# Performance work log

Hardware: AMD Instinct MI355X
Metric: run time of the kernel (lower is better)

The kernel has to match this reference:

```python
import jax, jax.numpy as jnp
import numpy as np

TOP_K = 30
NUM_RBF = 16
MAXREL = 32


def _normalize(x, eps=1e-12):
    return x / jnp.maximum(jnp.linalg.norm(x, axis=-1, keepdims=True), eps)


def gather_edges(edges, idx):
    # edges [B,L,L,C], idx [B,L,K] -> [B,L,K,C]
    return jnp.take_along_axis(edges, idx[..., None], axis=2)


def gather_nodes(nodes, idx):
    # nodes [B,L,C], idx [B,L,K] -> [B,L,K,C]
    B, L, K = idx.shape
    flat = idx.reshape(B, L * K)
    g = jnp.take_along_axis(nodes, flat[:, :, None], axis=1)
    return g.reshape(B, L, K, nodes.shape[-1])


def _rbf(D):
    mu = jnp.linspace(2.0, 22.0, NUM_RBF)
    sigma = (22.0 - 2.0) / NUM_RBF
    return jnp.exp(-(((D[..., None] - mu) / sigma) ** 2))


def _get_rbf(A, B, E_idx):
    D = jnp.sqrt(jnp.sum((A[:, :, None, :] - B[:, None, :, :]) ** 2, -1) + 1e-6)
    Dn = gather_edges(D[..., None], E_idx)[..., 0]
    return _rbf(Dn)


def _dist(X, mask, eps=1e-6):
    mask2 = mask[:, None, :] * mask[:, :, None]
    dX = X[:, None, :, :] - X[:, :, None, :]
    D = mask2 * jnp.sqrt(jnp.sum(dX ** 2, -1) + eps)
    D_max = jnp.max(D, -1, keepdims=True)
    D_adjust = D + (1.0 - mask2) * D_max
    k = min(TOP_K, X.shape[1])
    neg_vals, E_idx = jax.lax.top_k(-D_adjust, k)  # smallest-k distances
    D_neighbors = -neg_vals
    mask_neighbors = gather_edges(mask2[..., None], E_idx)
    return D_neighbors, E_idx, mask_neighbors


def _quaternions(R):
    # R [B,L,K,3,3] -> Q [B,L,K,4]
    diag = jnp.diagonal(R, axis1=-2, axis2=-1)
    Rxx, Ryy, Rzz = diag[..., 0], diag[..., 1], diag[..., 2]
    magnitudes = 0.5 * jnp.sqrt(jnp.abs(1.0 + jnp.stack(
        [Rxx - Ryy - Rzz, -Rxx + Ryy - Rzz, -Rxx - Ryy + Rzz], -1)))
    signs = jnp.sign(jnp.stack([
        R[..., 2, 1] - R[..., 1, 2],
        R[..., 0, 2] - R[..., 2, 0],
        R[..., 1, 0] - R[..., 0, 1]], -1))
    xyz = signs * magnitudes
    w = jnp.sqrt(jax.nn.relu(1.0 + jnp.sum(diag, -1, keepdims=True))) / 2.0
    Q = jnp.concatenate((xyz, w), -1)
    return _normalize(Q)


def _orientations_coarse(X, E_idx, eps=1e-6):
    dX = X[:, 1:, :] - X[:, :-1, :]
    dX_norm = jnp.linalg.norm(dX, axis=-1)
    dX_mask = ((dX_norm > 3.6) & (dX_norm < 4.0)).astype(X.dtype)
    dX = dX * dX_mask[:, :, None]
    U = _normalize(dX)
    u_2, u_1, u_0 = U[:, :-2, :], U[:, 1:-1, :], U[:, 2:, :]
    n_2 = _normalize(jnp.cross(u_2, u_1))
    n_1 = _normalize(jnp.cross(u_1, u_0))
    cosA = jnp.clip(-(u_1 * u_0).sum(-1), -1 + eps, 1 - eps)
    A = jnp.arccos(cosA)
    cosD = jnp.clip((n_2 * n_1).sum(-1), -1 + eps, 1 - eps)
    Dang = jnp.sign((u_2 * n_1).sum(-1)) * jnp.arccos(cosD)
    AD = jnp.stack((jnp.cos(A), jnp.sin(A) * jnp.cos(Dang),
                    jnp.sin(A) * jnp.sin(Dang)), -1)
    AD = jnp.pad(AD, ((0, 0), (1, 2), (0, 0)))  # [B,L,3]
    o_1 = _normalize(u_2 - u_1)
    O = jnp.stack((o_1, n_2, jnp.cross(o_1, n_2)), -2)  # [B,L-3,3,3]
    O = O.reshape(O.shape[0], O.shape[1], 9)
    O = jnp.pad(O, ((0, 0), (1, 2), (0, 0)))  # [B,L,9]
    O_nb = gather_nodes(O, E_idx).reshape(E_idx.shape[0], E_idx.shape[1], E_idx.shape[2], 3, 3)
    X_nb = gather_nodes(X, E_idx)
    Om = O.reshape(O.shape[0], O.shape[1], 3, 3)
    dXn = X_nb - X[:, :, None, :]
    dU = _normalize(jnp.einsum('blij,blkj->blki', Om, dXn))
    R = jnp.einsum('blji,blkjm->blkim', Om, O_nb)  # O^T @ O_neighbors
    Q = _quaternions(R)
    return AD, jnp.concatenate((dU, Q), -1)  # [B,L,3], [B,L,K,7]


def _forward(Ca, mask, residue_idx, chain_labels, pos_W, pos_b, edge_W, ln_g, ln_b):
    D_neighbors, E_idx, mask_neighbors = _dist(Ca, mask)
    Ca_0 = jnp.pad(Ca[:, :-1, :], ((0, 0), (1, 0), (0, 0)))
    Ca_1 = Ca
    Ca_2 = jnp.pad(Ca[:, 1:, :], ((0, 0), (0, 1), (0, 0)))
    V, O_features = _orientations_coarse(Ca, E_idx)
    RBF_all = jnp.concatenate([
        _rbf(D_neighbors),
        _get_rbf(Ca_0, Ca_0, E_idx),
        _get_rbf(Ca_2, Ca_2, E_idx),
        _get_rbf(Ca_0, Ca_1, E_idx),
        _get_rbf(Ca_0, Ca_2, E_idx),
        _get_rbf(Ca_1, Ca_0, E_idx),
        _get_rbf(Ca_1, Ca_2, E_idx),
        _get_rbf(Ca_2, Ca_0, E_idx),
        _get_rbf(Ca_2, Ca_1, E_idx)], -1)  # [B,L,K,144]
    offset = residue_idx[:, :, None] - residue_idx[:, None, :]
    offset = gather_edges(offset[..., None], E_idx)[..., 0]
    d_chains = (chain_labels[:, :, None] - chain_labels[:, None, :] == 0).astype(jnp.int32)
    E_chains = gather_edges(d_chains[..., None], E_idx)[..., 0]
    d = jnp.clip(offset + MAXREL, 0, 2 * MAXREL) * E_chains + (1 - E_chains) * (2 * MAXREL + 1)
    d_onehot = jax.nn.one_hot(d, 2 * MAXREL + 2, dtype=pos_W.dtype)
    E_positional = d_onehot @ pos_W + pos_b
    E = jnp.concatenate((E_positional, RBF_all, O_features), -1)  # [B,L,K,167]
    E = E @ edge_W  # no bias
    mu = jnp.mean(E, -1, keepdims=True)
    var = jnp.var(E, -1, keepdims=True)
    E = (E - mu) / jnp.sqrt(var + 1e-5) * ln_g + ln_b
    return E, E_idx


def setup_inputs() -> dict:
    key = jax.random.key(0)
    k1, k2, k3 = jax.random.split(key, 3)
    B, L = 2, 4096
    Ca = jax.random.normal(k1, (B, L, 3), dtype=jnp.float32) * 10.0
    mask = jnp.ones((B, L), dtype=jnp.float32)
    residue_idx = jnp.arange(B * L, dtype=jnp.int32).reshape(B, L) % L
    chain_labels = jnp.zeros((B, L), dtype=jnp.int32)
    pos_W = jax.random.normal(k2, (2 * MAXREL + 2, 16), dtype=jnp.float32) * 0.1
    pos_b = jnp.zeros((16,), dtype=jnp.float32)
    edge_in = 16 + NUM_RBF * 9 + 7  # 167
    edge_W = jax.random.normal(k3, (edge_in, 128), dtype=jnp.float32) * 0.05
    ln_g = jnp.ones((128,), dtype=jnp.float32)
    ln_b = jnp.zeros((128,), dtype=jnp.float32)
    return {"Ca": Ca, "mask": mask, "residue_idx": residue_idx,
            "chain_labels": chain_labels, "pos_W": pos_W, "pos_b": pos_b,
            "edge_W": edge_W, "ln_g": ln_g, "ln_b": ln_b}


def reference(Ca, mask, residue_idx, chain_labels, pos_W, pos_b, edge_W, ln_g, ln_b):
    return _forward(Ca, mask, residue_idx, chain_labels, pos_W, pos_b, edge_W, ln_g, ln_b)
```

## Files before the change

### kernel.cpp

```cpp
#include <hip/hip_runtime.h>
#include <math.h>

constexpr int Lc   = 4096;
constexpr int Bc   = 2;
constexpr int KNB  = 30;
constexpr int NF   = 167;
constexpr int NC   = 128;
constexpr int KP   = 200;
constexpr int NKT  = 6;
constexpr int CAP  = 512;

typedef __attribute__((ext_vector_type(8))) short bf16x8;
typedef __attribute__((ext_vector_type(4))) float f32x4;

struct V3 { float x, y, z; };

__device__ __forceinline__ float sgnf(float v) {
    return (v > 0.f) ? 1.f : ((v < 0.f) ? -1.f : 0.f);
}
__device__ __forceinline__ unsigned long long umin64(unsigned long long a, unsigned long long b) {
    return a < b ? a : b;
}
__device__ __forceinline__ void splitbf(float v, unsigned short& h, unsigned short& l) {
    unsigned u = __float_as_uint(v);
    h = (unsigned short)(u >> 16);
    float fh = __uint_as_float((unsigned)h << 16);
    l = (unsigned short)(__float_as_uint(v - fh) >> 16);
}
__device__ __forceinline__ unsigned cvtpk(float a, float b) {
    unsigned r;
    asm("v_cvt_pk_bf16_f32 %0, %1, %2" : "=v"(r) : "v"(a), "v"(b));
    return r;
}

__device__ __forceinline__ V3 unit_seg(float dx, float dy, float dz) {
    float n = sqrtf(dx * dx + dy * dy + dz * dz);
    float m = (n > 3.6f && n < 4.0f) ? 1.f : 0.f;
    float nn = fmaxf(m * n, 1e-12f);
    V3 r; r.x = dx * m / nn; r.y = dy * m / nn; r.z = dz * m / nn;
    return r;
}

__global__ __launch_bounds__(256) void topk_prep_kernel(
    const float* __restrict__ Ca, const float* __restrict__ mask,
    float* __restrict__ EidxF, int* __restrict__ EidxI,
    float* __restrict__ O, const float* __restrict__ W,
    unsigned short* __restrict__ Wh, unsigned short* __restrict__ Wl,
    int rows) {
    const int t = threadIdx.x;

    if (blockIdx.x >= rows) {
        int pb = blockIdx.x - rows;
        if (pb < 32) {
            int idx = pb * 256 + t;
            if (idx >= Bc * Lc) return;
            int b = idx >> 12, l = idx & (Lc - 1);
            float* o = O + (size_t)idx * 9;
            if (l < 1 || l >= Lc - 2) {
#pragma unroll
                for (int q = 0; q < 9; ++q) o[q] = 0.f;
                return;
            }
            const float* C = Ca + ((size_t)b * Lc + (l - 1)) * 3;
            V3 u2 = unit_seg(C[3] - C[0], C[4] - C[1], C[5] - C[2]);
            V3 u1 = unit_seg(C[6] - C[3], C[7] - C[4], C[8] - C[5]);
            float nx = u2.y * u1.z - u2.z * u1.y;
            float ny = u2.z * u1.x - u2.x * u1.z;
            float nz = u2.x * u1.y - u2.y * u1.x;
            float nn = fmaxf(sqrtf(nx * nx + ny * ny + nz * nz), 1e-12f);
            nx /= nn; ny /= nn; nz /= nn;
            float ox = u2.x - u1.x, oy = u2.y - u1.y, oz = u2.z - u1.z;
            float on = fmaxf(sqrtf(ox * ox + oy * oy + oz * oz), 1e-12f);
            ox /= on; oy /= on; oz /= on;
            o[0] = ox; o[1] = oy; o[2] = oz;
            o[3] = nx; o[4] = ny; o[5] = nz;
            o[6] = oy * nz - oz * ny;
            o[7] = oz * nx - ox * nz;
            o[8] = ox * ny - oy * nx;
        } else {
            int tt = (pb - 32) * 256 + t;
            if (tt >= NKT * 8 * 64) return;
            int lane = tt & 63, nt = (tt >> 6) & 7, kt = tt >> 9;
            int n = nt * 16 + (lane & 15);
            int kbase = kt * 32 + (lane >> 4) * 8;
            __align__(16) unsigned short h[8], l[8];
#pragma unroll
            for (int j = 0; j < 8; ++j) {
                int k = kbase + j;
                float v = (k < NF) ? W[(size_t)k * NC + n] : 0.f;
                splitbf(v, h[j], l[j]);
            }
            size_t o = (size_t)tt * 8;
            *(bf16x8*)(Wh + o) = *(const bf16x8*)h;
            *(bf16x8*)(Wl + o) = *(const bf16x8*)l;
        }
        return;
    }

    const int row = blockIdx.x;
    const int b = row >> 12, i = row & (Lc - 1);
    const float* CaB = Ca + (size_t)b * Lc * 3;
    const float* mB  = mask + (size_t)b * Lc;
    const float xi = CaB[i * 3 + 0], yi = CaB[i * 3 + 1], zi = CaB[i * 3 + 2];
    const float mi = mB[i];

    __shared__ unsigned long long cand[CAP];
    __shared__ float redf[4];
    __shared__ int redi[2][4];
    __shared__ int redi4[4][4];
    __shared__ int candN;

    const int lane = t & 63, wid = t >> 6;
    if (t == 0) candN = 0;

    float ss[16], m2a[16];
    float lmax = -1e30f;
#pragma unroll
    for (int k = 0; k < 16; ++k) {
        int j = t + k * 256;
        float dx = CaB[j * 3 + 0] - xi;
        float dy = CaB[j * 3 + 1] - yi;
        float dz = CaB[j * 3 + 2] - zi;
        float s = dx * dx + dy * dy + dz * dz;
        float m2 = mi * mB[j];
        float v = m2 * s;
        ss[k] = v; m2a[k] = m2;
        lmax = fmaxf(lmax, v);
    }
    for (int off = 32; off; off >>= 1) lmax = fmaxf(lmax, __shfl_xor(lmax, off));
    if (lane == 0) redf[wid] = lmax;
    __syncthreads();
    const float ssmax = fmaxf(fmaxf(redf[0], redf[1]), fmaxf(redf[2], redf[3]));

#pragma unroll
    for (int k = 0; k < 16; ++k) ss[k] = ss[k] + (1.f - m2a[k]) * ssmax;

    const float Tb = ssmax * 0.037772f;
    float T;
    int c;
    {
        const float t0 = Tb, t1 = Tb * 3.f, t2 = Tb * 9.f, t3 = Tb * 27.f;
        int l0 = 0, l1 = 0, l2 = 0, l3 = 0;
#pragma unroll
        for (int k = 0; k < 16; ++k) {
            float v = ss[k];
            l0 += (v <= t0) ? 1 : 0;
            l1 += (v <= t1) ? 1 : 0;
            l2 += (v <= t2) ? 1 : 0;
            l3 += (v <= t3) ? 1 : 0;
        }
        for (int off = 32; off; off >>= 1) {
            l0 += __shfl_xor(l0, off); l1 += __shfl_xor(l1, off);
            l2 += __shfl_xor(l2, off); l3 += __shfl_xor(l3, off);
        }
        if (lane == 0) {
            redi4[wid][0] = l0; redi4[wid][1] = l1;
            redi4[wid][2] = l2; redi4[wid][3] = l3;
        }
        __syncthreads();
        int c0 = redi4[0][0] + redi4[1][0] + redi4[2][0] + redi4[3][0];
        int c1 = redi4[0][1] + redi4[1][1] + redi4[2][1] + redi4[3][1];
        int c2 = redi4[0][2] + redi4[1][2] + redi4[2][2] + redi4[3][2];
        int c3 = redi4[0][3] + redi4[1][3] + redi4[2][3] + redi4[3][3];
        if (c0 >= KNB)      { T = t0; c = c0; }
        else if (c1 >= KNB) { T = t1; c = c1; }
        else if (c2 >= KNB) { T = t2; c = c2; }
        else                { T = t3; c = c3; }
    }

    for (int iter = 1; iter < 32; ++iter) {
        if (c >= KNB && c <= 64) break;
        if (iter >= 12 && c >= KNB && c <= CAP) break;
        if (c < KNB) {
            if (c == 0) T *= 2.89f;
            else {
                float f = cbrtf((float)(KNB + 15) / (float)c);
                T *= fminf(2.89f, 1.1025f * f * f);
            }
        } else {
            float f = cbrtf(45.f / (float)c);
            T *= fmaxf(0.3025f, 1.1025f * f * f);
        }
        int lc = 0;
#pragma unroll
        for (int k = 0; k < 16; ++k) lc += (ss[k] <= T) ? 1 : 0;
        for (int off = 32; off; off >>= 1) lc += __shfl_xor(lc, off);
        if (lane == 0) redi[iter & 1][wid] = lc;
        __syncthreads();
        c = redi[iter & 1][0] + redi[iter & 1][1] + redi[iter & 1][2] + redi[iter & 1][3];
    }

#pragma unroll
    for (int k = 0; k < 16; ++k) {
        if (ss[k] <= T) {
            int idx = atomicAdd(&candN, 1);
            if (idx < CAP)
                cand[idx] = ((unsigned long long)__float_as_uint(ss[k]) << 32) |
                            (unsigned)(t + k * 256);
        }
    }
    __syncthreads();

    if (wid == 0) {
        int C = candN; if (C > CAP) C = CAP;
        if (C <= 64) {
            unsigned long long key = (lane < C) ? cand[lane] : ~0ULL;
#pragma unroll
            for (int size = 2; size <= 64; size <<= 1) {
#pragma unroll
                for (int stride = size >> 1; stride; stride >>= 1) {
                    unsigned long long other = __shfl_xor(key, stride);
                    bool dirUp = ((lane & size) == 0);
                    bool takeMin = ((lane & stride) == 0) ? dirUp : !dirUp;
                    bool less = other < key;
                    unsigned long long mn = less ? other : key;
                    unsigned long long mx = less ? key : other;
                    key = takeMin ? mn : mx;
                }
            }
            if (lane < KNB) {
                int jw = (int)(key & 0xFFFFFFFFULL);
                EidxF[(size_t)row * KNB + lane] = (float)jw;
                EidxI[(size_t)row * KNB + lane] = jw;
            }
        } else {
            unsigned long long r[CAP / 64];
#pragma unroll
            for (int q = 0; q < CAP / 64; ++q) {
                int idx = lane + q * 64;
                r[q] = (idx < C) ? cand[idx] : ~0ULL;
            }
            for (int p = 0; p < KNB; ++p) {
                unsigned long long mn = r[0];
#pragma unroll
                for (int q = 1; q < CAP / 64; ++q) mn = umin64(mn, r[q]);
                for (int off = 32; off; off >>= 1) mn = umin64(mn, __shfl_xor(mn, off));
                if (lane == 0) {
                    int jw = (int)(mn & 0xFFFFFFFFULL);
                    EidxF[(size_t)row * KNB + p] = (float)jw;
                    EidxI[(size_t)row * KNB + p] = jw;
                }
#pragma unroll
                for (int q = 0; q < CAP / 64; ++q) if (r[q] == mn) r[q] = ~0ULL;
            }
        }
    }
}

__global__ __launch_bounds__(256) void edge_kernel(
    const float* __restrict__ Ca, const int* __restrict__ ridx,
    const int* __restrict__ clab, const float* __restrict__ pos_W,
    const float* __restrict__ pos_b,
    const unsigned short* __restrict__ Wh, const unsigned short* __restrict__ Wl,
    const float* __restrict__ ln_g, const float* __restrict__ ln_b,
    const int* __restrict__ EidxI, const float* __restrict__ Omat,
    float* __restrict__ outE) {
    const int row = blockIdx.x;
    const int b = row >> 12, i = row & (Lc - 1);
    const int tid = threadIdx.x, lane = tid & 63, w = tid >> 6;

    __shared__ __align__(16) unsigned short Fh[32][KP];
    __shared__ float Ssum[32][4];
    __shared__ float Ssq[32][4];
    __shared__ float2 Mstat[32];
    __shared__ int Ej[32];
    __shared__ float Cnb[32 * 13];
    __shared__ float Cis[12];

    const float* CaB = Ca + (size_t)b * Lc * 3;

    if (tid < KNB) Ej[tid] = EidxI[(size_t)row * KNB + tid];
    for (int q = tid; q < 32 * 33; q += 256) {
        int r = q / 33, c = 167 + q % 33;
        Fh[r][c] = 0;
    }
    for (int q = tid; q < 2 * 167; q += 256) {
        int r = 30 + q / 167, c = q % 167;
        Fh[r][c] = 0;
    }
    __syncthreads();

    if (tid < 90) {
        int e = tid / 3, p = tid % 3;
        int n = Ej[e] - 1 + p;
        float x = 0.f, y = 0.f, z = 0.f;
        if (n >= 0 && n < Lc) { x = CaB[n*3]; y = CaB[n*3+1]; z = CaB[n*3+2]; }
        Cnb[e * 13 + p * 3 + 0] = x;
        Cnb[e * 13 + p * 3 + 1] = y;
        Cnb[e * 13 + p * 3 + 2] = z;
    } else if (tid >= 96 && tid < 99) {
        int p = tid - 96;
        int n = i - 1 + p;
        float x = 0.f, y = 0.f, z = 0.f;
        if (n >= 0 && n < Lc) { x = CaB[n*3]; y = CaB[n*3+1]; z = CaB[n*3+2]; }
        Cis[p * 4 + 0] = x; Cis[p * 4 + 1] = y; Cis[p * 4 + 2] = z;
    }
    __syncthreads();

    auto putF2 = [&](int e, int k, float va, float vb) {
        *(unsigned*)&Fh[e][k] = cvtpk(va, vb);
    };
    auto ldNb = [&](int e, int p) {
        V3 r; r.x = Cnb[e * 13 + p * 3 + 0];
        r.y = Cnb[e * 13 + p * 3 + 1];
        r.z = Cnb[e * 13 + p * 3 + 2];
        return r;
    };
    auto ldI = [&](int p) {
        V3 r; r.x = Cis[p * 4 + 0]; r.y = Cis[p * 4 + 1]; r.z = Cis[p * 4 + 2];
        return r;
    };

    auto rbf_task = [&](int r) {
        int e = r % 30, g = r / 30 + 1;
        int pa = (int)((0xA5084u >> (2 * g)) & 3u);
        int pb = (int)((0x48984u >> (2 * g)) & 3u);
        V3 A = ldI(pa);
        V3 B = ldNb(e, pb);
        float dx = A.x - B.x, dy = A.y - B.y, dz = A.z - B.z;
        float D8 = sqrtf(dx * dx + dy * dy + dz * dz + 1e-6f) * (1.f / 1.25f);
        int k0 = 16 * g;
#pragma unroll
        for (int m = 0; m < 16; m += 2) {
            float z0 = D8 - (2.f + (20.f / 15.f) * (float)m) * (1.f / 1.25f);
            float z1 = D8 - (2.f + (20.f / 15.f) * (float)(m + 1)) * (1.f / 1.25f);
            putF2(e, k0 + m, __expf(-z0 * z0), __expf(-z1 * z1));
        }
    };

    rbf_task(tid);

    if (w == 0) {
        if (lane < 14) rbf_task(256 + lane);
    } else if (w == 1) {
        if (lane < KNB) {
            int e = lane, j = Ej[e];
            int off = ridx[(size_t)b * Lc + i] - ridx[(size_t)b * Lc + j];
            int ec = (clab[(size_t)b * Lc + i] == clab[(size_t)b * Lc + j]) ? 1 : 0;
            int d = ec ? min(max(off + 32, 0), 64) : 65;
#pragma unroll
            for (int cc = 0; cc < 16; cc += 2)
                putF2(e, cc, pos_W[d * 16 + cc] + pos_b[cc],
                             pos_W[d * 16 + cc + 1] + pos_b[cc + 1]);
        }
    } else if (w == 2) {
        if (lane < KNB) {
            int e = lane, j = Ej[e];
            const float* Om = Omat + (size_t)row * 9;
            const float* On = Omat + ((size_t)b * Lc + j) * 9;
            V3 Ai = ldI(1), Bj = ldNb(e, 1);
            float dvx = Bj.x - Ai.x, dvy = Bj.y - Ai.y, dvz = Bj.z - Ai.z;
            float u0 = Om[0] * dvx + Om[1] * dvy + Om[2] * dvz;
            float u1 = Om[3] * dvx + Om[4] * dvy + Om[5] * dvz;
            float u2 = Om[6] * dvx + Om[7] * dvy + Om[8] * dvz;
            float un = fmaxf(sqrtf(u0 * u0 + u1 * u1 + u2 * u2), 1e-12f);
            float R[3][3];
#pragma unroll
            for (int a = 0; a < 3; ++a)
#pragma unroll
                for (int m = 0; m < 3; ++m)
                    R[a][m] = Om[0 * 3 + a] * On[0 * 3 + m] +
                              Om[1 * 3 + a] * On[1 * 3 + m] +
                              Om[2 * 3 + a] * On[2 * 3 + m];
            float Rxx = R[0][0], Ryy = R[1][1], Rzz = R[2][2];
            float m0 = 0.5f * sqrtf(fabsf(1.f + Rxx - Ryy - Rzz));
            float m1 = 0.5f * sqrtf(fabsf(1.f - Rxx + Ryy - Rzz));
            float m2 = 0.5f * sqrtf(fabsf(1.f - Rxx - Ryy + Rzz));
            float qx = sgnf(R[2][1] - R[1][2]) * m0;
            float qy = sgnf(R[0][2] - R[2][0]) * m1;
            float qz = sgnf(R[1][0] - R[0][1]) * m2;
            float qw = sqrtf(fmaxf(0.f, 1.f + Rxx + Ryy + Rzz)) * 0.5f;
            float qn = fmaxf(sqrtf(qx * qx + qy * qy + qz * qz + qw * qw), 1e-12f);
            putF2(e, 160, u0 / un, u1 / un);
            putF2(e, 162, u2 / un, qx / qn);
            putF2(e, 164, qy / qn, qz / qn);
            putF2(e, 166, qw / qn, 0.f);
        }
    }
    __syncthreads();

    const int arow = lane & 15, agrp = lane >> 4;
    const int ng0 = w * 2;
    f32x4 acc[2][2];
#pragma unroll
    for (int m = 0; m < 2; ++m)
#pragma unroll
        for (int n = 0; n < 2; ++n) acc[m][n] = (f32x4){0.f, 0.f, 0.f, 0.f};

    const bf16x8* WhF = (const bf16x8*)Wh;
    const bf16x8* WlF = (const bf16x8*)Wl;

#pragma unroll
    for (int kt = 0; kt < NKT; ++kt) {
        const int kof = kt * 32 + agrp * 8;
        bf16x8 a0 = *(const bf16x8*)&Fh[arow][kof];
        bf16x8 a1 = *(const bf16x8*)&Fh[16 + arow][kof];
        bf16x8 b0h = WhF[(kt * 8 + ng0) * 64 + lane];
        bf16x8 b1h = WhF[(kt * 8 + ng0 + 1) * 64 + lane];
        bf16x8 b0l = WlF[(kt * 8 + ng0) * 64 + lane];
        bf16x8 b1l = WlF[(kt * 8 + ng0 + 1) * 64 + lane];

        acc[0][0] = __builtin_amdgcn_mfma_f32_16x16x32_bf16(a0, b0h, acc[0][0], 0, 0, 0);
        acc[0][0] = __builtin_amdgcn_mfma_f32_16x16x32_bf16(a0, b0l, acc[0][0], 0, 0, 0);
        acc[0][1] = __builtin_amdgcn_mfma_f32_16x16x32_bf16(a0, b1h, acc[0][1], 0, 0, 0);
        acc[0][1] = __builtin_amdgcn_mfma_f32_16x16x32_bf16(a0, b1l, acc[0][1], 0, 0, 0);
        acc[1][0] = __builtin_amdgcn_mfma_f32_16x16x32_bf16(a1, b0h, acc[1][0], 0, 0, 0);
        acc[1][0] = __builtin_amdgcn_mfma_f32_16x16x32_bf16(a1, b0l, acc[1][0], 0, 0, 0);
        acc[1][1] = __builtin_amdgcn_mfma_f32_16x16x32_bf16(a1, b1h, acc[1][1], 0, 0, 0);
        acc[1][1] = __builtin_amdgcn_mfma_f32_16x16x32_bf16(a1, b1l, acc[1][1], 0, 0, 0);
    }

    float ps[2][4], pq[2][4];
#pragma unroll
    for (int m = 0; m < 2; ++m)
#pragma unroll
        for (int r = 0; r < 4; ++r) {
            float v0 = acc[m][0][r], v1 = acc[m][1][r];
            ps[m][r] = v0 + v1;
            pq[m][r] = v0 * v0 + v1 * v1;
        }
#pragma unroll
    for (int off = 1; off < 16; off <<= 1) {
#pragma unroll
        for (int m = 0; m < 2; ++m)
#pragma unroll
            for (int r = 0; r < 4; ++r) {
                ps[m][r] += __shfl_xor(ps[m][r], off);
                pq[m][r] += __shfl_xor(pq[m][r], off);
            }
    }
    if (arow == 0) {
#pragma unroll
        for (int m = 0; m < 2; ++m)
#pragma unroll
            for (int r = 0; r < 4; ++r) {
                int me = m * 16 + agrp * 4 + r;
                Ssum[me][w] = ps[m][r];
                Ssq[me][w] = pq[m][r];
            }
    }
    __syncthreads();
    if (tid < 32) {
        float s = Ssum[tid][0] + Ssum[tid][1] + Ssum[tid][2] + Ssum[tid][3];
        float q = Ssq[tid][0] + Ssq[tid][1] + Ssq[tid][2] + Ssq[tid][3];
        float mean = s * (1.f / 128.f);
        float var = q * (1.f / 128.f) - mean * mean;
        Mstat[tid] = make_float2(mean, 1.f / sqrtf(var + 1e-5f));
    }
    __syncthreads();

    float gg[2], bb[2];
#pragma unroll
    for (int n = 0; n < 2; ++n) {
        int ce = (ng0 + n) * 16 + arow;
        gg[n] = ln_g[ce];
        bb[n] = ln_b[ce];
    }
#pragma unroll
    for (int m = 0; m < 2; ++m)
#pragma unroll
        for (int r = 0; r < 4; ++r) {
            int me = m * 16 + agrp * 4 + r;
            if (me >= KNB) continue;
            float2 st = Mstat[me];
            size_t base = ((size_t)row * KNB + me) * NC;
#pragma unroll
            for (int n = 0; n < 2; ++n) {
                int ce = (ng0 + n) * 16 + arow;
                outE[base + ce] = (acc[m][n][r] - st.x) * st.y * gg[n] + bb[n];
            }
        }
}

extern "C" void kernel_launch(void* const* d_in, const int* in_sizes, int n_in,
                              void* d_out, int out_size, void* d_ws, size_t ws_size,
                              hipStream_t stream) {
    const float* Ca     = (const float*)d_in[0];
    const float* mask   = (const float*)d_in[1];
    const int*   ridx   = (const int*)d_in[2];
    const int*   clab   = (const int*)d_in[3];
    const float* pos_W  = (const float*)d_in[4];
    const float* pos_b  = (const float*)d_in[5];
    const float* edge_W = (const float*)d_in[6];
    const float* ln_g   = (const float*)d_in[7];
    const float* ln_b   = (const float*)d_in[8];

    float* outE  = (float*)d_out;
    float* EidxF = outE + (size_t)Bc * Lc * KNB * NC;

    float* Omat  = (float*)d_ws;
    int*   EidxI = (int*)(Omat + (size_t)Bc * Lc * 9);
    unsigned short* Wh = (unsigned short*)(EidxI + (size_t)Bc * Lc * KNB);
    unsigned short* Wl = Wh + (size_t)NKT * 8 * 64 * 8;

    const int rows = Bc * Lc;
    topk_prep_kernel<<<rows + 44, 256, 0, stream>>>(Ca, mask, EidxF, EidxI,
                                                    Omat, edge_W, Wh, Wl, rows);
    edge_kernel<<<rows, 256, 0, stream>>>(Ca, ridx, clab, pos_W, pos_b, Wh, Wl,
                                          ln_g, ln_b, EidxI, Omat, outE);
}
```

Baseline: 116.1 us.

## Process two residue rows per edge_kernel block to reuse weight fragments

Each edge_kernel block now handles two consecutive rows, 60 edges padded to 64, instead of one row padded to 32. The same B-operand weight fragments loaded from global memory feed twice as many MFMAs, and per-block setup and synchronisation are amortised over more work. Shared memory and accumulator registers roughly double and the grid halves, which may lower occupancy or parallelism.

```diff
diff --git a/kernel.cpp b/kernel.cpp
--- a/kernel.cpp
+++ b/kernel.cpp
@@ -9,6 +9,7 @@
 constexpr int KP   = 200;
 constexpr int NKT  = 6;
 constexpr int CAP  = 512;
+constexpr int NE   = 60;
 
 typedef __attribute__((ext_vector_type(8))) short bf16x8;
 typedef __attribute__((ext_vector_type(4))) float f32x4;
@@ -255,32 +256,35 @@
     const float* __restrict__ ln_g, const float* __restrict__ ln_b,
     const int* __restrict__ EidxI, const float* __restrict__ Omat,
     float* __restrict__ outE) {
-    const int row = blockIdx.x;
-    const int b = row >> 12, i = row & (Lc - 1);
+    const int r0 = blockIdx.x * 2;
+    const int b = r0 >> 12, i0 = r0 & (Lc - 1);
     const int tid = threadIdx.x, lane = tid & 63, w = tid >> 6;
 
-    __shared__ __align__(16) unsigned short Fh[32][KP];
-    __shared__ float Ssum[32][4];
-    __shared__ float Ssq[32][4];
-    __shared__ float2 Mstat[32];
-    __shared__ int Ej[32];
-    __shared__ float Cnb[32 * 13];
-    __shared__ float Cis[12];
+    __shared__ __align__(16) unsigned short Fh[64][KP];
+    __shared__ float Ssum[64][4];
+    __shared__ float Ssq[64][4];
+    __shared__ float2 Mstat[64];
+    __shared__ int Ej[64];
+    __shared__ float Cnb[NE * 13];
+    __shared__ float Cis[16];
 
     const float* CaB = Ca + (size_t)b * Lc * 3;
 
-    if (tid < KNB) Ej[tid] = EidxI[(size_t)row * KNB + tid];
-    for (int q = tid; q < 32 * 33; q += 256) {
+    if (tid < NE) {
+        int rr = r0 + (tid >= KNB ? 1 : 0);
+        Ej[tid] = EidxI[(size_t)rr * KNB + (tid % KNB)];
+    }
+    for (int q = tid; q < 64 * 33; q += 256) {
         int r = q / 33, c = 167 + q % 33;
         Fh[r][c] = 0;
     }
-    for (int q = tid; q < 2 * 167; q += 256) {
-        int r = 30 + q / 167, c = q % 167;
+    for (int q = tid; q < 4 * 167; q += 256) {
+        int r = 60 + q / 167, c = q % 167;
         Fh[r][c] = 0;
     }
     __syncthreads();
 
-    if (tid < 90) {
+    if (tid < NE * 3) {
         int e = tid / 3, p = tid % 3;
         int n = Ej[e] - 1 + p;
         float x = 0.f, y = 0.f, z = 0.f;
@@ -288,9 +292,9 @@
         Cnb[e * 13 + p * 3 + 0] = x;
         Cnb[e * 13 + p * 3 + 1] = y;
         Cnb[e * 13 + p * 3 + 2] = z;
-    } else if (tid >= 96 && tid < 99) {
-        int p = tid - 96;
-        int n = i - 1 + p;
+    } else if (tid >= 192 && tid < 196) {
+        int p = tid - 192;
+        int n = i0 - 1 + p;
         float x = 0.f, y = 0.f, z = 0.f;
         if (n >= 0 && n < Lc) { x = CaB[n*3]; y = CaB[n*3+1]; z = CaB[n*3+2]; }
         Cis[p * 4 + 0] = x; Cis[p * 4 + 1] = y; Cis[p * 4 + 2] = z;
@@ -312,8 +316,8 @@
     };
 
     auto rbf_task = [&](int r) {
-        int e = r % 30, g = r / 30 + 1;
-        int pa = (int)((0xA5084u >> (2 * g)) & 3u);
+        int e = r % NE, g = r / NE + 1;
+        int pa = (int)((0xA5084u >> (2 * g)) & 3u) + (e >= KNB ? 1 : 0);
         int pb = (int)((0x48984u >> (2 * g)) & 3u);
         V3 A = ldI(pa);
         V3 B = ldNb(e, pb);
@@ -329,14 +333,16 @@
     };
 
     rbf_task(tid);
+    rbf_task(tid + 256);
 
     if (w == 0) {
-        if (lane < 14) rbf_task(256 + lane);
+        if (lane < 540 - 512) rbf_task(512 + lane);
     } else if (w == 1) {
-        if (lane < KNB) {
+        if (lane < NE) {
             int e = lane, j = Ej[e];
-            int off = ridx[(size_t)b * Lc + i] - ridx[(size_t)b * Lc + j];
-            int ec = (clab[(size_t)b * Lc + i] == clab[(size_t)b * Lc + j]) ? 1 : 0;
+            int ii = (e < KNB) ? i0 : i0 + 1;
+            int off = ridx[(size_t)b * Lc + ii] - ridx[(size_t)b * Lc + j];
+            int ec = (clab[(size_t)b * Lc + ii] == clab[(size_t)b * Lc + j]) ? 1 : 0;
             int d = ec ? min(max(off + 32, 0), 64) : 65;
 #pragma unroll
             for (int cc = 0; cc < 16; cc += 2)
@@ -344,11 +350,12 @@
                              pos_W[d * 16 + cc + 1] + pos_b[cc + 1]);
         }
     } else if (w == 2) {
-        if (lane < KNB) {
+        if (lane < NE) {
             int e = lane, j = Ej[e];
-            const float* Om = Omat + (size_t)row * 9;
+            int ii = (e < KNB) ? i0 : i0 + 1;
+            const float* Om = Omat + ((size_t)b * Lc + ii) * 9;
             const float* On = Omat + ((size_t)b * Lc + j) * 9;
-            V3 Ai = ldI(1), Bj = ldNb(e, 1);
+            V3 Ai = ldI((e < KNB) ? 1 : 2), Bj = ldNb(e, 1);
             float dvx = Bj.x - Ai.x, dvy = Bj.y - Ai.y, dvz = Bj.z - Ai.z;
             float u0 = Om[0] * dvx + Om[1] * dvy + Om[2] * dvz;
             float u1 = Om[3] * dvx + Om[4] * dvy + Om[5] * dvz;
@@ -381,9 +388,9 @@
 
     const int arow = lane & 15, agrp = lane >> 4;
     const int ng0 = w * 2;
-    f32x4 acc[2][2];
-#pragma unroll
-    for (int m = 0; m < 2; ++m)
+    f32x4 acc[4][2];
+#pragma unroll
+    for (int m = 0; m < 4; ++m)
 #pragma unroll
         for (int n = 0; n < 2; ++n) acc[m][n] = (f32x4){0.f, 0.f, 0.f, 0.f};
 
@@ -395,6 +402,8 @@
         const int kof = kt * 32 + agrp * 8;
         bf16x8 a0 = *(const bf16x8*)&Fh[arow][kof];
         bf16x8 a1 = *(const bf16x8*)&Fh[16 + arow][kof];
+        bf16x8 a2 = *(const bf16x8*)&Fh[32 + arow][kof];
+        bf16x8 a3 = *(const bf16x8*)&Fh[48 + arow][kof];
         bf16x8 b0h = WhF[(kt * 8 + ng0) * 64 + lane];
         bf16x8 b1h = WhF[(kt * 8 + ng0 + 1) * 64 + lane];
         bf16x8 b0l = WlF[(kt * 8 + ng0) * 64 + lane];
@@ -408,11 +417,19 @@
         acc[1][0] = __builtin_amdgcn_mfma_f32_16x16x32_bf16(a1, b0l, acc[1][0], 0, 0, 0);
         acc[1][1] = __builtin_amdgcn_mfma_f32_16x16x32_bf16(a1, b1h, acc[1][1], 0, 0, 0);
         acc[1][1] = __builtin_amdgcn_mfma_f32_16x16x32_bf16(a1, b1l, acc[1][1], 0, 0, 0);
-    }
-
-    float ps[2][4], pq[2][4];
-#pragma unroll
-    for (int m = 0; m < 2; ++m)
+        acc[2][0] = __builtin_amdgcn_mfma_f32_16x16x32_bf16(a2, b0h, acc[2][0], 0, 0, 0);
+        acc[2][0] = __builtin_amdgcn_mfma_f32_16x16x32_bf16(a2, b0l, acc[2][0], 0, 0, 0);
+        acc[2][1] = __builtin_amdgcn_mfma_f32_16x16x32_bf16(a2, b1h, acc[2][1], 0, 0, 0);
+        acc[2][1] = __builtin_amdgcn_mfma_f32_16x16x32_bf16(a2, b1l, acc[2][1], 0, 0, 0);
+        acc[3][0] = __builtin_amdgcn_mfma_f32_16x16x32_bf16(a3, b0h, acc[3][0], 0, 0, 0);
+        acc[3][0] = __builtin_amdgcn_mfma_f32_16x16x32_bf16(a3, b0l, acc[3][0], 0, 0, 0);
+        acc[3][1] = __builtin_amdgcn_mfma_f32_16x16x32_bf16(a3, b1h, acc[3][1], 0, 0, 0);
+        acc[3][1] = __builtin_amdgcn_mfma_f32_16x16x32_bf16(a3, b1l, acc[3][1], 0, 0, 0);
+    }
+
+    float ps[4][4], pq[4][4];
+#pragma unroll
+    for (int m = 0; m < 4; ++m)
 #pragma unroll
         for (int r = 0; r < 4; ++r) {
             float v0 = acc[m][0][r], v1 = acc[m][1][r];
@@ -422,7 +439,7 @@
 #pragma unroll
     for (int off = 1; off < 16; off <<= 1) {
 #pragma unroll
-        for (int m = 0; m < 2; ++m)
+        for (int m = 0; m < 4; ++m)
 #pragma unroll
             for (int r = 0; r < 4; ++r) {
                 ps[m][r] += __shfl_xor(ps[m][r], off);
@@ -431,7 +448,7 @@
     }
     if (arow == 0) {
 #pragma unroll
-        for (int m = 0; m < 2; ++m)
+        for (int m = 0; m < 4; ++m)
 #pragma unroll
             for (int r = 0; r < 4; ++r) {
                 int me = m * 16 + agrp * 4 + r;
@@ -440,7 +457,7 @@
             }
     }
     __syncthreads();
-    if (tid < 32) {
+    if (tid < 64) {
         float s = Ssum[tid][0] + Ssum[tid][1] + Ssum[tid][2] + Ssum[tid][3];
         float q = Ssq[tid][0] + Ssq[tid][1] + Ssq[tid][2] + Ssq[tid][3];
         float mean = s * (1.f / 128.f);
@@ -457,13 +474,15 @@
         bb[n] = ln_b[ce];
     }
 #pragma unroll
-    for (int m = 0; m < 2; ++m)
+    for (int m = 0; m < 4; ++m)
 #pragma unroll
         for (int r = 0; r < 4; ++r) {
             int me = m * 16 + agrp * 4 + r;
-            if (me >= KNB) continue;
+            if (me >= NE) continue;
+            int rr = r0 + (me >= KNB ? 1 : 0);
+            int eg = me % KNB;
             float2 st = Mstat[me];
-            size_t base = ((size_t)row * KNB + me) * NC;
+            size_t base = ((size_t)rr * KNB + eg) * NC;
 #pragma unroll
             for (int n = 0; n < 2; ++n) {
                 int ce = (ng0 + n) * 16 + arow;
@@ -496,6 +515,6 @@
     const int rows = Bc * Lc;
     topk_prep_kernel<<<rows + 44, 256, 0, stream>>>(Ca, mask, EidxF, EidxI,
                                                     Omat, edge_W, Wh, Wl, rows);
-    edge_kernel<<<rows, 256, 0, stream>>>(Ca, ridx, clab, pos_W, pos_b, Wh, Wl,
-                                          ln_g, ln_b, EidxI, Omat, outE);
-}
+    edge_kernel<<<rows / 2, 256, 0, stream>>>(Ca, ridx, clab, pos_W, pos_b, Wh, Wl,
+                                              ln_g, ln_b, EidxI, Omat, outE);
+}
```

Result: no change. 118.3 us (+1.9%).
